# Kernel tuning notes

Measured on AMD Instinct MI355X. Metric: run time of the kernel, lower is better.

The kernel has to match this reference:

```python
import jax, jax.numpy as jnp
import numpy as np

TOP_K = 6  # num_experts_per_tok


def _glu_mlp(x, wg, wu, wd):
    # DeepSeek MLP: down( silu(gate(x)) * up(x) )
    return (jax.nn.silu(x @ wg) * (x @ wu)) @ wd


def setup_inputs() -> dict:
    key = jax.random.key(0)
    ks = jax.random.split(key, 8)
    B, S, D, E, F, FS = 2, 2048, 1024, 8, 512, 1024
    sc = 0.02
    return {
        "hidden_states": jax.random.normal(ks[0], (B, S, D), jnp.float32),
        "router_w": jax.random.normal(ks[1], (D, E), jnp.float32) * sc,
        "w_gate": jax.random.normal(ks[2], (E, D, F), jnp.float32) * sc,
        "w_up": jax.random.normal(ks[3], (E, D, F), jnp.float32) * sc,
        "w_down": jax.random.normal(ks[4], (E, F, D), jnp.float32) * sc,
        "ws_gate": jax.random.normal(ks[5], (D, FS), jnp.float32) * sc,
        "ws_up": jax.random.normal(ks[6], (D, FS), jnp.float32) * sc,
        "ws_down": jax.random.normal(ks[7], (FS, D), jnp.float32) * sc,
    }


def reference(hidden_states, router_w, w_gate, w_up, w_down, ws_gate, ws_up, ws_down):
    B, S, D = hidden_states.shape
    x = hidden_states.reshape(-1, D)                       # [T, D] tokens
    # Gate: softmax router + top-k (DeepSeek gate, no renorm)
    scores = jax.nn.softmax(x @ router_w, axis=-1)         # [T, E]
    topk_w, topk_idx = jax.lax.top_k(scores, TOP_K)        # [T, K]
    # Expert SiLU-GLU MLPs evaluated for all experts (math-identical to the
    # argsort dispatch -> grouped GEMM -> scatter combine in moe_infer)
    g = jnp.einsum('td,edf->etf', x, w_gate)               # [E, T, F]
    u = jnp.einsum('td,edf->etf', x, w_up)                 # [E, T, F]
    f_all = jnp.einsum('etf,efd->ted', jax.nn.silu(g) * u, w_down)  # [T, E, D]
    # Combine: final[t] = sum_k topk_w[t,k] * expert_{topk_idx[t,k]}(x[t])
    picked = jnp.take_along_axis(f_all, topk_idx[:, :, None], axis=1)  # [T, K, D]
    y = jnp.sum(picked * topk_w[:, :, None], axis=1).reshape(B, S, D)
    # shared experts branch
    y = y + _glu_mlp(hidden_states, ws_gate, ws_up, ws_down)
    return y
```

## Files before the change

kernel.cpp:

```cpp
#include <hip/hip_runtime.h>

typedef __attribute__((ext_vector_type(8))) short bf16x8;
typedef __attribute__((ext_vector_type(4))) float floatx4;

static __device__ __forceinline__ float b2f(unsigned short u) {
  union { unsigned int i; float f; } v; v.i = ((unsigned int)u) << 16; return v.f;
}
static __device__ __forceinline__ unsigned short f2b(float f) {
  union { float f; unsigned int i; } v; v.f = f;
  unsigned int x = v.i;
  return (unsigned short)((x + 0x7fffu + ((x >> 16) & 1u)) >> 16);
}

#define GLDS(gp, lp) \
  __builtin_amdgcn_global_load_lds( \
      (const __attribute__((address_space(1))) unsigned int*)(gp), \
      (__attribute__((address_space(3))) unsigned int*)(lp), 16, 0, 0)

static __device__ __forceinline__ void swizzle_mn(int lin, int Mb, int Nb,
                                                  int& m_idx, int& n_idx) {
  if ((Mb & 7) == 0) {
    int xcd = lin & 7;
    int idx = lin >> 3;
    int nstrips = Mb >> 3;
    m_idx = (idx % nstrips) * 8 + xcd;
    n_idx = idx / nstrips;
  } else {
    m_idx = lin % Mb;
    n_idx = lin / Mb;
  }
}

__global__ void cvt_f32_bf16(const float* __restrict__ src,
                             unsigned short* __restrict__ dst) {
  int i = (blockIdx.x * 256 + threadIdx.x) * 4;
  float4 v = *(const float4*)(src + i);
  ushort4 o;
  o.x = f2b(v.x); o.y = f2b(v.y); o.z = f2b(v.z); o.w = f2b(v.w);
  *(ushort4*)(dst + i) = o;
}

__global__ void transpose_f32_bf16_2(const float* __restrict__ sA,
                                     unsigned short* __restrict__ dA, int nzA,
                                     const float* __restrict__ sB,
                                     unsigned short* __restrict__ dB,
                                     int K, int N) {
  __shared__ unsigned short tile[32][33];
  int z = blockIdx.z;
  const float* src;
  unsigned short* dst;
  if (z < nzA) { src = sA + (size_t)z * K * N; dst = dA + (size_t)z * K * N; }
  else { src = sB + (size_t)(z - nzA) * K * N; dst = dB + (size_t)(z - nzA) * K * N; }
  const int bx = blockIdx.x * 32;
  const int by = blockIdx.y * 32;
  const int tx = threadIdx.x, ty = threadIdx.y;
#pragma unroll
  for (int i = 0; i < 4; i++)
    tile[ty + i * 8][tx] = f2b(src[(size_t)(by + ty + i * 8) * N + bx + tx]);
  __syncthreads();
#pragma unroll
  for (int i = 0; i < 4; i++)
    dst[(size_t)(bx + ty + i * 8) * K + by + tx] = tile[tx][ty + i * 8];
}

__global__ void transpose3_1024(const float* __restrict__ s0,
                                const float* __restrict__ s1,
                                const float* __restrict__ s2,
                                unsigned short* __restrict__ d0,
                                unsigned short* __restrict__ d1,
                                unsigned short* __restrict__ d2) {
  __shared__ unsigned short tile[32][33];
  const float* src = (blockIdx.z == 0) ? s0 : (blockIdx.z == 1) ? s1 : s2;
  unsigned short* dst = (blockIdx.z == 0) ? d0 : (blockIdx.z == 1) ? d1 : d2;
  const int bx = blockIdx.x * 32;
  const int by = blockIdx.y * 32;
  const int tx = threadIdx.x, ty = threadIdx.y;
#pragma unroll
  for (int i = 0; i < 4; i++)
    tile[ty + i * 8][tx] = f2b(src[(size_t)(by + ty + i * 8) * 1024 + bx + tx]);
  __syncthreads();
#pragma unroll
  for (int i = 0; i < 4; i++)
    dst[(size_t)(bx + ty + i * 8) * 1024 + by + tx] = tile[tx][ty + i * 8];
}

__global__ void router_topk(const float* __restrict__ X,
                            const float* __restrict__ RW,
                            float* __restrict__ cw) {
  const int t = blockIdx.x;
  const int lane = threadIdx.x;
  float acc[8];
#pragma unroll
  for (int e = 0; e < 8; e++) acc[e] = 0.f;
  for (int d = lane; d < 1024; d += 64) {
    float xv = X[(size_t)t * 1024 + d];
    const float* r = RW + d * 8;
    float4 r0 = *(const float4*)r;
    float4 r1 = *(const float4*)(r + 4);
    acc[0] += xv * r0.x; acc[1] += xv * r0.y;
    acc[2] += xv * r0.z; acc[3] += xv * r0.w;
    acc[4] += xv * r1.x; acc[5] += xv * r1.y;
    acc[6] += xv * r1.z; acc[7] += xv * r1.w;
  }
#pragma unroll
  for (int m = 1; m < 64; m <<= 1) {
#pragma unroll
    for (int e = 0; e < 8; e++) acc[e] += __shfl_xor(acc[e], m);
  }
  if (lane == 0) {
    float mx = acc[0];
#pragma unroll
    for (int e = 1; e < 8; e++) mx = fmaxf(mx, acc[e]);
    float prob[8], s = 0.f;
#pragma unroll
    for (int e = 0; e < 8; e++) { prob[e] = expf(acc[e] - mx); s += prob[e]; }
    float inv = 1.f / s;
#pragma unroll
    for (int e = 0; e < 8; e++) prob[e] *= inv;
    int m1 = 0;
#pragma unroll
    for (int e = 1; e < 8; e++) if (prob[e] < prob[m1]) m1 = e;
    int m2 = -1;
#pragma unroll
    for (int e = 0; e < 8; e++)
      if (e != m1 && (m2 < 0 || prob[e] < prob[m2])) m2 = e;
#pragma unroll
    for (int e = 0; e < 8; e++)
      cw[(size_t)t * 8 + e] = (e == m1 || e == m2) ? 0.f : prob[e];
  }
}

__global__ __launch_bounds__(256) void gemm_gu_fused(
    const unsigned short* __restrict__ X,
    const unsigned short* __restrict__ WgTe,
    const unsigned short* __restrict__ WgTs,
    const unsigned short* __restrict__ WuTe,
    const unsigned short* __restrict__ WuTs,
    unsigned short* __restrict__ H,
    const float* __restrict__ cw, int Mb) {
  __shared__ __align__(16) unsigned short lA[128 * 32];
  __shared__ __align__(16) unsigned short lBg[64 * 32];
  __shared__ __align__(16) unsigned short lBu[64 * 32];
  const int tid = threadIdx.x;
  const int wid = tid >> 6, lane = tid & 63;
  const int lr = lane & 15, quad = lane >> 4;
  const int wm = wid >> 1, wn = wid & 1;
  int m_idx, n_idx;
  swizzle_mn(blockIdx.x, Mb, 80, m_idx, n_idx);
  const int m0 = m_idx * 128;
  const int n0 = n_idx * 64;

  const unsigned short *Bg, *Bu;
  int eidx = -1;
  if (n0 < 4096) {
    eidx = n0 >> 9;
    size_t off = ((size_t)eidx * 512 + (n0 & 511)) * 1024;
    Bg = WgTe + off; Bu = WuTe + off;
  } else {
    size_t off = (size_t)(n0 - 4096) * 1024;
    Bg = WgTs + off; Bu = WuTs + off;
  }

  floatx4 ag[4][2], au[4][2];
#pragma unroll
  for (int i = 0; i < 4; i++)
#pragma unroll
    for (int j = 0; j < 2; j++) { ag[i][j] = (floatx4)0.f; au[i][j] = (floatx4)0.f; }

  for (int k0 = 0; k0 < 1024; k0 += 32) {
    __syncthreads();
    {
#pragma unroll
      for (int i = 0; i < 2; i++) {
        int c = i * 256 + tid;
        int row = c >> 2;
        int g = ((c & 3) ^ ((row >> 1) & 3)) << 3;
        GLDS(X + (size_t)(m0 + row) * 1024 + k0 + g,
             lA + (size_t)(i * 256 + wid * 64) * 8);
      }
      int c = tid;
      int row = c >> 2;
      int g = ((c & 3) ^ ((row >> 1) & 3)) << 3;
      GLDS(Bg + (size_t)row * 1024 + k0 + g, lBg + (size_t)(wid * 64) * 8);
      GLDS(Bu + (size_t)row * 1024 + k0 + g, lBu + (size_t)(wid * 64) * 8);
    }
    __syncthreads();
    bf16x8 af[4], bg[2], bu[2];
#pragma unroll
    for (int mt = 0; mt < 4; mt++) {
      int row = wm * 64 + mt * 16 + lr;
      af[mt] = *(const bf16x8*)(lA + row * 32 + ((quad ^ ((row >> 1) & 3)) << 3));
    }
#pragma unroll
    for (int nt = 0; nt < 2; nt++) {
      int row = wn * 32 + nt * 16 + lr;
      int o = row * 32 + ((quad ^ ((row >> 1) & 3)) << 3);
      bg[nt] = *(const bf16x8*)(lBg + o);
      bu[nt] = *(const bf16x8*)(lBu + o);
    }
#pragma unroll
    for (int mt = 0; mt < 4; mt++)
#pragma unroll
      for (int nt = 0; nt < 2; nt++) {
        ag[mt][nt] = __builtin_amdgcn_mfma_f32_16x16x32_bf16(
            af[mt], bg[nt], ag[mt][nt], 0, 0, 0);
        au[mt][nt] = __builtin_amdgcn_mfma_f32_16x16x32_bf16(
            af[mt], bu[nt], au[mt][nt], 0, 0, 0);
      }
  }

#pragma unroll
  for (int mt = 0; mt < 4; mt++) {
#pragma unroll
    for (int nt = 0; nt < 2; nt++) {
#pragma unroll
      for (int r = 0; r < 4; r++) {
        int row = m0 + wm * 64 + mt * 16 + quad * 4 + r;
        int col = n0 + wn * 32 + nt * 16 + lr;
        float g = ag[mt][nt][r];
        float u = au[mt][nt][r];
        float s = (eidx >= 0) ? cw[(size_t)row * 8 + eidx] : 1.0f;
        float silu = g / (1.0f + __expf(-g));
        H[(size_t)row * 5120 + col] = f2b(s * silu * u);
      }
    }
  }
}

__global__ __launch_bounds__(256) void gemm_down(
    const unsigned short* __restrict__ H,
    const unsigned short* __restrict__ WdTe,
    const unsigned short* __restrict__ WdTs,
    float* __restrict__ Y, int Mb) {
  __shared__ __align__(16) unsigned short lA[128 * 64];
  __shared__ __align__(16) unsigned short lB[64 * 64];
  const int tid = threadIdx.x;
  const int wid = tid >> 6, lane = tid & 63;
  const int lr = lane & 15, quad = lane >> 4;
  const int wm = wid >> 1, wn = wid & 1;
  int m_idx, n_idx;
  swizzle_mn(blockIdx.x, Mb, 16, m_idx, n_idx);
  const int m0 = m_idx * 128;
  const int n0 = n_idx * 64;

  floatx4 acc[4][2];
#pragma unroll
  for (int i = 0; i < 4; i++)
#pragma unroll
    for (int j = 0; j < 2; j++) acc[i][j] = (floatx4)0.f;

  for (int k0 = 0; k0 < 5120; k0 += 64) {
    __syncthreads();
#pragma unroll
    for (int i = 0; i < 4; i++) {
      int c = i * 256 + tid;
      int row = c >> 3;
      int g = ((c & 7) ^ (row & 7)) << 3;
      GLDS(H + (size_t)(m0 + row) * 5120 + k0 + g,
           lA + (size_t)(i * 256 + wid * 64) * 8);
    }
#pragma unroll
    for (int i = 0; i < 2; i++) {
      int c = i * 256 + tid;
      int row = c >> 3;
      int g = ((c & 7) ^ (row & 7)) << 3;
      const unsigned short* gpb;
      if (k0 < 4096) {
        gpb = WdTe + (size_t)(k0 >> 9) * (1024 * 512) +
              (size_t)(n0 + row) * 512 + (k0 & 511) + g;
      } else {
        gpb = WdTs + (size_t)(n0 + row) * 1024 + (k0 - 4096) + g;
      }
      GLDS(gpb, lB + (size_t)(i * 256 + wid * 64) * 8);
    }
    __syncthreads();
    bf16x8 af[4][2], bfr[2][2];
#pragma unroll
    for (int mt = 0; mt < 4; mt++) {
      int row = wm * 64 + mt * 16 + lr;
#pragma unroll
      for (int kt = 0; kt < 2; kt++)
        af[mt][kt] = *(const bf16x8*)(lA + row * 64 +
                                      ((((kt << 2) + quad) ^ (row & 7)) << 3));
    }
#pragma unroll
    for (int nt = 0; nt < 2; nt++) {
      int row = wn * 32 + nt * 16 + lr;
#pragma unroll
      for (int kt = 0; kt < 2; kt++)
        bfr[nt][kt] = *(const bf16x8*)(lB + row * 64 +
                                       ((((kt << 2) + quad) ^ (row & 7)) << 3));
    }
#pragma unroll
    for (int kt = 0; kt < 2; kt++)
#pragma unroll
      for (int mt = 0; mt < 4; mt++)
#pragma unroll
        for (int nt = 0; nt < 2; nt++)
          acc[mt][nt] = __builtin_amdgcn_mfma_f32_16x16x32_bf16(
              af[mt][kt], bfr[nt][kt], acc[mt][nt], 0, 0, 0);
  }

#pragma unroll
  for (int mt = 0; mt < 4; mt++)
#pragma unroll
    for (int nt = 0; nt < 2; nt++)
#pragma unroll
      for (int r = 0; r < 4; r++) {
        int row = m0 + wm * 64 + mt * 16 + quad * 4 + r;
        int col = n0 + wn * 32 + nt * 16 + lr;
        Y[(size_t)row * 1024 + col] = acc[mt][nt][r];
      }
}

extern "C" void kernel_launch(void* const* d_in, const int* in_sizes, int n_in,
                              void* d_out, int out_size, void* d_ws, size_t ws_size,
                              hipStream_t stream) {
  const float* hs  = (const float*)d_in[0];
  const float* rw  = (const float*)d_in[1];
  const float* wg  = (const float*)d_in[2];
  const float* wu  = (const float*)d_in[3];
  const float* wd  = (const float*)d_in[4];
  const float* wsg = (const float*)d_in[5];
  const float* wsu = (const float*)d_in[6];
  const float* wsd = (const float*)d_in[7];
  float* out = (float*)d_out;

  char* p = (char*)d_ws;
  float* cw = (float*)p;                    p += (size_t)4096 * 8 * 4;
  unsigned short* Xb   = (unsigned short*)p; p += (size_t)4096 * 1024 * 2;
  unsigned short* wgT  = (unsigned short*)p; p += (size_t)8 * 512 * 1024 * 2;
  unsigned short* wuT  = (unsigned short*)p; p += (size_t)8 * 512 * 1024 * 2;
  unsigned short* wsgT = (unsigned short*)p; p += (size_t)1024 * 1024 * 2;
  unsigned short* wsuT = (unsigned short*)p; p += (size_t)1024 * 1024 * 2;
  unsigned short* wdT  = (unsigned short*)p; p += (size_t)8 * 1024 * 512 * 2;
  unsigned short* wsdT = (unsigned short*)p; p += (size_t)1024 * 1024 * 2;
  unsigned short* GH   = (unsigned short*)p;
  const size_t base_bytes = (size_t)(p - (char*)d_ws);

  int chunks = 8;
  for (int c = 1; c <= 8; c *= 2) {
    size_t gh_bytes = ((size_t)4096 / c) * 5120 * 2;
    if (base_bytes + gh_bytes <= ws_size) { chunks = c; break; }
  }
  const int rows = 4096 / chunks;
  const int Mb = rows / 128;

  dim3 tb(32, 8);
  cvt_f32_bf16<<<4096, 256, 0, stream>>>(hs, Xb);
  router_topk<<<4096, 64, 0, stream>>>(hs, rw, cw);
  transpose_f32_bf16_2<<<dim3(16, 32, 16), tb, 0, stream>>>(
      wg, wgT, 8, wu, wuT, 1024, 512);
  transpose_f32_bf16_2<<<dim3(32, 16, 8), tb, 0, stream>>>(
      wd, wdT, 8, wd, wdT, 512, 1024);
  transpose3_1024<<<dim3(32, 32, 3), tb, 0, stream>>>(
      wsg, wsu, wsd, wsgT, wsuT, wsdT);

  for (int c = 0; c < chunks; c++) {
    const unsigned short* Xc = Xb + (size_t)c * rows * 1024;
    const float* cwc = cw + (size_t)c * rows * 8;
    float* outc = out + (size_t)c * rows * 1024;
    gemm_gu_fused<<<Mb * 80, 256, 0, stream>>>(
        Xc, wgT, wsgT, wuT, wsuT, GH, cwc, Mb);
    gemm_down<<<Mb * 16, 256, 0, stream>>>(GH, wdT, wsdT, outc, Mb);
  }
}
```

Measured before the change: 311.3 us.

## Rewrite gate/up GEMM with 256x128 tiles and double-buffered LDS pipeline

The fused gate/up GEMM moves from 128x64 tiles with 256 threads to 256x128 tiles with 512 threads. It uses a K step of 64 and a double-buffered 128KB LDS, with interleaved global-to-LDS prefetch stages, explicit vmcnt waits and raw barriers, plus setprio around the MFMA blocks. The intent is to raise arithmetic intensity per loaded byte and overlap global loads with MFMA work, cutting the per-iteration sync and load stalls of the old single-buffer loop. The cost is a large LDS footprint per block, which limits occupancy, and hand-tuned wait counts that must stay correct. Grid swizzling is also changed to match the larger tiles.

```diff
diff --git a/kernel.cpp b/kernel.cpp
--- a/kernel.cpp
+++ b/kernel.cpp
@@ -130,7 +130,52 @@
   }
 }
 
-__global__ __launch_bounds__(256) void gemm_gu_fused(
+#define VMCNT(N) asm volatile("s_waitcnt vmcnt(" #N ")" ::: "memory")
+#define BARS() do { __builtin_amdgcn_s_barrier(); \
+                    __builtin_amdgcn_sched_barrier(0); } while (0)
+
+#define STG_I0(K, BS) do { \
+  GLDS(a0 + (K),          sm + (BS) + wid * 512); \
+  GLDS(a0 + (K) + 131072, sm + (BS) + 8192 + wid * 512); } while (0)
+#define STG_I1(K, BS) do { \
+  GLDS(bg0 + (K),        sm + (BS) + 16384 + wid * 1024); \
+  GLDS(bg0 + (K) + 8192, sm + (BS) + 16384 + wid * 1024 + 512); } while (0)
+#define STG_I2(K, BS) do { \
+  GLDS(bu0 + (K),        sm + (BS) + 24576 + wid * 1024); \
+  GLDS(bu0 + (K) + 8192, sm + (BS) + 24576 + wid * 1024 + 512); } while (0)
+#define STG_I3(K, BS) do { \
+  GLDS(a0 + (K) + 65536,  sm + (BS) + 4096 + wid * 512); \
+  GLDS(a0 + (K) + 196608, sm + (BS) + 12288 + wid * 512); } while (0)
+
+#define READ_A(DST, DB, H) do { _Pragma("unroll") \
+  for (int mf = 0; mf < 4; ++mf) { \
+    const int row_ = wm * 128 + (H) * 64 + mf * 16 + lr; \
+    const int rb_ = (DB) + row_ * 64; const int rx_ = row_ & 7; \
+    DST[mf][0] = *(const bf16x8*)(sm + rb_ + ((quad ^ rx_) << 3)); \
+    DST[mf][1] = *(const bf16x8*)(sm + rb_ + (((4 + quad) ^ rx_) << 3)); \
+  } } while (0)
+
+#define READ_B(DST, DB, RG) do { _Pragma("unroll") \
+  for (int nf = 0; nf < 2; ++nf) { \
+    const int row_ = wn * 32 + nf * 16 + lr; \
+    const int rb_ = (DB) + (RG) + row_ * 64; const int rx_ = row_ & 7; \
+    DST[nf][0] = *(const bf16x8*)(sm + rb_ + ((quad ^ rx_) << 3)); \
+    DST[nf][1] = *(const bf16x8*)(sm + rb_ + (((4 + quad) ^ rx_) << 3)); \
+  } } while (0)
+
+#define MM(ACC, AF, BF) do { \
+  __builtin_amdgcn_s_setprio(1); \
+  _Pragma("unroll") \
+  for (int mf = 0; mf < 4; ++mf) { _Pragma("unroll") \
+    for (int nf = 0; nf < 2; ++nf) { \
+      ACC[mf][nf] = __builtin_amdgcn_mfma_f32_16x16x32_bf16( \
+          AF[mf][0], BF[nf][0], ACC[mf][nf], 0, 0, 0); \
+      ACC[mf][nf] = __builtin_amdgcn_mfma_f32_16x16x32_bf16( \
+          AF[mf][1], BF[nf][1], ACC[mf][nf], 0, 0, 0); \
+    } } \
+  __builtin_amdgcn_s_setprio(0); } while (0)
+
+__global__ __launch_bounds__(512, 2) void gemm_gu_fused(
     const unsigned short* __restrict__ X,
     const unsigned short* __restrict__ WgTe,
     const unsigned short* __restrict__ WgTs,
@@ -138,17 +183,26 @@
     const unsigned short* __restrict__ WuTs,
     unsigned short* __restrict__ H,
     const float* __restrict__ cw, int Mb) {
-  __shared__ __align__(16) unsigned short lA[128 * 32];
-  __shared__ __align__(16) unsigned short lBg[64 * 32];
-  __shared__ __align__(16) unsigned short lBu[64 * 32];
+  __shared__ __align__(16) unsigned short sm[65536];
   const int tid = threadIdx.x;
   const int wid = tid >> 6, lane = tid & 63;
   const int lr = lane & 15, quad = lane >> 4;
-  const int wm = wid >> 1, wn = wid & 1;
+  const int wm = wid >> 2, wn = wid & 3;
+
   int m_idx, n_idx;
-  swizzle_mn(blockIdx.x, Mb, 80, m_idx, n_idx);
-  const int m0 = m_idx * 128;
-  const int n0 = n_idx * 64;
+  {
+    int lin = blockIdx.x;
+    if ((Mb & 7) == 0) {
+      int xcd = lin & 7, idx = lin >> 3;
+      n_idx = idx % 40;
+      m_idx = (idx / 40) * 8 + xcd;
+    } else {
+      m_idx = lin % Mb;
+      n_idx = lin / Mb;
+    }
+  }
+  const int m0 = m_idx * 256;
+  const int n0 = n_idx * 128;
 
   const unsigned short *Bg, *Bu;
   int eidx = -1;
@@ -161,67 +215,82 @@
     Bg = WgTs + off; Bu = WuTs + off;
   }
 
-  floatx4 ag[4][2], au[4][2];
-#pragma unroll
-  for (int i = 0; i < 4; i++)
-#pragma unroll
-    for (int j = 0; j < 2; j++) { ag[i][j] = (floatx4)0.f; au[i][j] = (floatx4)0.f; }
-
-  for (int k0 = 0; k0 < 1024; k0 += 32) {
-    __syncthreads();
-    {
-#pragma unroll
-      for (int i = 0; i < 2; i++) {
-        int c = i * 256 + tid;
-        int row = c >> 2;
-        int g = ((c & 3) ^ ((row >> 1) & 3)) << 3;
-        GLDS(X + (size_t)(m0 + row) * 1024 + k0 + g,
-             lA + (size_t)(i * 256 + wid * 64) * 8);
+  const int grow8 = lane >> 3;
+  const int gcol = ((lane & 7) ^ grow8) << 3;
+  const unsigned short* a0 =
+      X + (size_t)(m0 + wid * 8 + grow8) * 1024 + gcol;
+  const unsigned short* bg0 =
+      Bg + (size_t)(wid * 16 + grow8) * 1024 + gcol;
+  const unsigned short* bu0 =
+      Bu + (size_t)(wid * 16 + grow8) * 1024 + gcol;
+
+  floatx4 gg[2][4][2], uu[2][4][2];
+#pragma unroll
+  for (int h = 0; h < 2; h++)
+#pragma unroll
+    for (int mf = 0; mf < 4; mf++)
+#pragma unroll
+      for (int nf = 0; nf < 2; nf++) {
+        gg[h][mf][nf] = (floatx4)0.f;
+        uu[h][mf][nf] = (floatx4)0.f;
       }
-      int c = tid;
-      int row = c >> 2;
-      int g = ((c & 3) ^ ((row >> 1) & 3)) << 3;
-      GLDS(Bg + (size_t)row * 1024 + k0 + g, lBg + (size_t)(wid * 64) * 8);
-      GLDS(Bu + (size_t)row * 1024 + k0 + g, lBu + (size_t)(wid * 64) * 8);
-    }
-    __syncthreads();
-    bf16x8 af[4], bg[2], bu[2];
-#pragma unroll
-    for (int mt = 0; mt < 4; mt++) {
-      int row = wm * 64 + mt * 16 + lr;
-      af[mt] = *(const bf16x8*)(lA + row * 32 + ((quad ^ ((row >> 1) & 3)) << 3));
-    }
-#pragma unroll
-    for (int nt = 0; nt < 2; nt++) {
-      int row = wn * 32 + nt * 16 + lr;
-      int o = row * 32 + ((quad ^ ((row >> 1) & 3)) << 3);
-      bg[nt] = *(const bf16x8*)(lBg + o);
-      bu[nt] = *(const bf16x8*)(lBu + o);
-    }
-#pragma unroll
-    for (int mt = 0; mt < 4; mt++)
-#pragma unroll
-      for (int nt = 0; nt < 2; nt++) {
-        ag[mt][nt] = __builtin_amdgcn_mfma_f32_16x16x32_bf16(
-            af[mt], bg[nt], ag[mt][nt], 0, 0, 0);
-        au[mt][nt] = __builtin_amdgcn_mfma_f32_16x16x32_bf16(
-            af[mt], bu[nt], au[mt][nt], 0, 0, 0);
-      }
-  }
-
-#pragma unroll
-  for (int mt = 0; mt < 4; mt++) {
-#pragma unroll
-    for (int nt = 0; nt < 2; nt++) {
-#pragma unroll
-      for (int r = 0; r < 4; r++) {
-        int row = m0 + wm * 64 + mt * 16 + quad * 4 + r;
-        int col = n0 + wn * 32 + nt * 16 + lr;
-        float g = ag[mt][nt][r];
-        float u = au[mt][nt][r];
-        float s = (eidx >= 0) ? cw[(size_t)row * 8 + eidx] : 1.0f;
-        float silu = g / (1.0f + __expf(-g));
-        H[(size_t)row * 5120 + col] = f2b(s * silu * u);
+
+  bf16x8 fA0[4][2], fA1[4][2], fBg[2][2], fBu[2][2];
+
+  STG_I0(0, 0); STG_I1(0, 0); STG_I2(0, 0); STG_I3(0, 0);
+
+  for (int t = 0; t < 15; ++t) {
+    const int db = (t & 1) << 15;
+    const int nb = 32768 - db;
+    const int kn = (t + 1) * 64;
+    STG_I0(kn, nb);
+    VMCNT(6); BARS();
+    READ_A(fA0, db, 0);
+    READ_B(fBg, db, 16384);
+    MM(gg[0], fA0, fBg);
+    STG_I1(kn, nb);
+    VMCNT(6); BARS();
+    READ_B(fBu, db, 24576);
+    MM(uu[0], fA0, fBu);
+    STG_I2(kn, nb);
+    VMCNT(6); BARS();
+    READ_A(fA1, db, 1);
+    MM(gg[1], fA1, fBg);
+    STG_I3(kn, nb);
+    BARS();
+    MM(uu[1], fA1, fBu);
+  }
+  {
+    const int db = 32768;
+    VMCNT(4); BARS();
+    READ_A(fA0, db, 0);
+    READ_B(fBg, db, 16384);
+    MM(gg[0], fA0, fBg);
+    VMCNT(2); BARS();
+    READ_B(fBu, db, 24576);
+    MM(uu[0], fA0, fBu);
+    VMCNT(0); BARS();
+    READ_A(fA1, db, 1);
+    MM(gg[1], fA1, fBg);
+    MM(uu[1], fA1, fBu);
+  }
+
+#pragma unroll
+  for (int h = 0; h < 2; h++) {
+#pragma unroll
+    for (int mf = 0; mf < 4; mf++) {
+#pragma unroll
+      for (int nf = 0; nf < 2; nf++) {
+#pragma unroll
+        for (int r = 0; r < 4; r++) {
+          int row = m0 + wm * 128 + h * 64 + mf * 16 + quad * 4 + r;
+          int col = n0 + wn * 32 + nf * 16 + lr;
+          float g = gg[h][mf][nf][r];
+          float u = uu[h][mf][nf][r];
+          float s = (eidx >= 0) ? cw[(size_t)row * 8 + eidx] : 1.0f;
+          float silu = g / (1.0f + __expf(-g));
+          H[(size_t)row * 5120 + col] = f2b(s * silu * u);
+        }
       }
     }
   }
@@ -345,6 +414,7 @@
   }
   const int rows = 4096 / chunks;
   const int Mb = rows / 128;
+  const int MbG = rows / 256;
 
   dim3 tb(32, 8);
   cvt_f32_bf16<<<4096, 256, 0, stream>>>(hs, Xb);
@@ -360,8 +430,8 @@
     const unsigned short* Xc = Xb + (size_t)c * rows * 1024;
     const float* cwc = cw + (size_t)c * rows * 8;
     float* outc = out + (size_t)c * rows * 1024;
-    gemm_gu_fused<<<Mb * 80, 256, 0, stream>>>(
-        Xc, wgT, wsgT, wuT, wsuT, GH, cwc, Mb);
+    gemm_gu_fused<<<MbG * 40, 512, 0, stream>>>(
+        Xc, wgT, wsgT, wuT, wsuT, GH, cwc, MbG);
     gemm_down<<<Mb * 16, 256, 0, stream>>>(GH, wdT, wsdT, outc, Mb);
   }
 }
```

After: 309.9 us. Within noise of the previous version (-0.4%).
